# Kernel tuning notes

Measured on AMD Instinct MI355X. Metric: run time of the kernel, lower is better.

## Reference

```python
import jax, jax.numpy as jnp
import numpy as np

B, NI, D, P, R = 32, 1024, 1024, 1000, 3  # batch, patches, d_model, pool_size, agg rounds


def setup_inputs() -> dict:
    key = jax.random.key(0)
    ks = jax.random.split(key, 12)
    w = lambda k, shape: jax.random.normal(k, shape, jnp.float32) * 0.02
    return {
        "att_feats": jax.random.normal(ks[0], (B, NI, D), jnp.float32),
        "fc_feats": jax.random.normal(ks[1], (B, D), jnp.float32),
        "pool": jax.random.normal(ks[2], (P, D), jnp.float32),
        "W_agg": w(ks[3], (R, D, D)),          # stacked agg projections (no bias)
        "Wq": w(ks[4], (D, D)), "bq": jnp.zeros((D,), jnp.float32),
        "Wk": w(ks[5], (D, D)), "bk": jnp.zeros((D,), jnp.float32),
        "Wv": w(ks[6], (D, D)), "bv": jnp.zeros((D,), jnp.float32),
        "Wc": w(ks[7], (D, D)), "bc": jnp.zeros((D,), jnp.float32),
        "Wg": w(ks[8], (2 * D,)), "bg": jnp.asarray(-1.0, jnp.float32),  # gate bias init -1
        "residual_scale": jnp.asarray(0.1, jnp.float32),
    }


def reference(att_feats, fc_feats, pool, W_agg, Wq, bq, Wk, bk, Wv, bv, Wc, bc, Wg, bg, residual_scale):
    d = att_feats.shape[-1]
    scale = 1.0 / jnp.sqrt(jnp.asarray(d, att_feats.dtype))
    v_hat = fc_feats  # fc dim == d_model path

    # Aggregate attention: R rounds over normality pool, averaged (Eq. 4-6)
    q_all = jnp.einsum('bd,rod->rbo', v_hat, W_agg)            # [R,B,D]
    scores = jnp.einsum('rbo,po->rbp', q_all, pool) * scale    # [R,B,P]
    weights = jax.nn.softmax(scores, axis=-1)
    v_agg = jnp.einsum('rbp,pd->bd', weights, pool) / R        # [B,D]

    # Differentiate attention (Eq. 7-10)
    q = v_hat @ Wq.T + bq
    k = v_agg @ Wk.T + bk
    v = v_agg @ Wv.T + bv
    sim = jnp.sum(q * k, axis=-1, keepdims=True) * scale       # [B,1]
    v_common = jax.nn.sigmoid(sim) * v
    v_diff = jax.nn.relu((v_hat - v_common) @ Wc.T + bc)       # [B,D] (dropout = identity, eval)

    # Gated residual; split gate weight to avoid materializing the concat
    Wg1, Wg2 = Wg[:d], Wg[d:]
    g = jax.nn.sigmoid(att_feats @ Wg1 + (v_diff @ Wg2)[:, None] + bg)  # [B,NI]
    return att_feats + residual_scale * g[..., None] * v_diff[:, None, :]
```

## Files before the change

### kernel.cpp

```cpp
#include <hip/hip_runtime.h>

#define D 1024
#define B 32
#define NI 1024
#define PP 1000
#define R 3
#define SPLITS 8
#define VS 8
#define BK 32
#define KT (D / SPLITS / BK)
#define PAD 34

typedef float f32x4_t __attribute__((ext_vector_type(4)));

__device__ __forceinline__ void nt_store4v(float* p, f32x4_t x) {
    __builtin_nontemporal_store(x, (f32x4_t*)p);
}

__device__ __forceinline__ float wred(float x) {
    #pragma unroll
    for (int off = 32; off; off >>= 1) x += __shfl_xor(x, off, 64);
    return x;
}
__device__ __forceinline__ float wmax(float x) {
    #pragma unroll
    for (int off = 32; off; off >>= 1) x = fmaxf(x, __shfl_xor(x, off, 64));
    return x;
}

template<int NXS>
__device__ __forceinline__ void gemm_core(
        const float* __restrict__ A, int mbase, int Mrows,
        const float* __restrict__ Xb, int xrstride, size_t xss,
        int kc0, float acc[4][4]) {
    __shared__ float Ws[128][PAD];
    __shared__ float Xs[32][PAD];
    const int t = threadIdx.x;
    const int ty = t >> 3, tx = t & 7;
    const int m0 = 4 * ty, b0 = 4 * tx;
    const int lrow = t >> 3, lq = t & 7;

    #pragma unroll
    for (int i = 0; i < 4; ++i)
        #pragma unroll
        for (int j = 0; j < 4; ++j) acc[i][j] = 0.f;

    for (int kt = 0; kt < KT; ++kt) {
        const int kc = kc0 + kt * BK;
        #pragma unroll
        for (int rr = 0; rr < 4; ++rr) {
            const int row = lrow + 32 * rr;
            float4 v = make_float4(0.f, 0.f, 0.f, 0.f);
            if (mbase + row < Mrows)
                v = *(const float4*)(A + (size_t)(mbase + row) * D + kc + 4 * lq);
            *(float2*)&Ws[row][4 * lq]     = make_float2(v.x, v.y);
            *(float2*)&Ws[row][4 * lq + 2] = make_float2(v.z, v.w);
        }
        {
            const float* xp = Xb + (size_t)lrow * xrstride + kc + 4 * lq;
            float4 v = *(const float4*)xp;
            #pragma unroll
            for (int s = 1; s < NXS; ++s) {
                float4 w = *(const float4*)(xp + (size_t)s * xss);
                v.x += w.x; v.y += w.y; v.z += w.z; v.w += w.w;
            }
            *(float2*)&Xs[lrow][4 * lq]     = make_float2(v.x, v.y);
            *(float2*)&Xs[lrow][4 * lq + 2] = make_float2(v.z, v.w);
        }
        __syncthreads();
        #pragma unroll
        for (int kp = 0; kp < 16; ++kp) {
            float2 wv[4], xv[4];
            #pragma unroll
            for (int i = 0; i < 4; ++i) wv[i] = *(const float2*)&Ws[m0 + i][2 * kp];
            #pragma unroll
            for (int j = 0; j < 4; ++j) xv[j] = *(const float2*)&Xs[b0 + j][2 * kp];
            #pragma unroll
            for (int i = 0; i < 4; ++i)
                #pragma unroll
                for (int j = 0; j < 4; ++j) {
                    acc[i][j] += wv[i].x * xv[j].x;
                    acc[i][j] += wv[i].y * xv[j].y;
                }
        }
        __syncthreads();
    }
}

__global__ __launch_bounds__(256) void gemm_k1q(const float* __restrict__ Wagg,
        const float* __restrict__ Wq, const float* __restrict__ fc,
        float* __restrict__ qallp, float* __restrict__ qkvp) {
    const int mb = blockIdx.x, s = blockIdx.y;
    const int t = threadIdx.x, ty = t >> 3, tx = t & 7;
    float acc[4][4];
    if (mb < 24) {
        const int mbase = mb * 128;
        gemm_core<1>(Wagg, mbase, R * D, fc, D, 0, s * 128, acc);
        const int m = mbase + 4 * ty;
        #pragma unroll
        for (int j = 0; j < 4; ++j) {
            float* cp = qallp + ((size_t)(s * B) + 4 * tx + j) * (R * D) + m;
            *(float4*)cp = make_float4(acc[0][j], acc[1][j], acc[2][j], acc[3][j]);
        }
    } else {
        const int mbase = (mb - 24) * 128;
        gemm_core<1>(Wq, mbase, D, fc, D, 0, s * 128, acc);
        const int m = mbase + 4 * ty;
        #pragma unroll
        for (int j = 0; j < 4; ++j) {
            float* cp = qkvp + ((size_t)((s * R + 0) * B) + 4 * tx + j) * D + m;
            *(float4*)cp = make_float4(acc[0][j], acc[1][j], acc[2][j], acc[3][j]);
        }
    }
}

__global__ __launch_bounds__(256) void gemm_k2(const float* __restrict__ pool,
        const float* __restrict__ qallp, float* __restrict__ Cp) {
    const int mb = blockIdx.x, s = blockIdx.y, r = blockIdx.z;
    const int mbase = mb * 128;
    float acc[4][4];
    gemm_core<SPLITS>(pool, mbase, PP, qallp + r * D, R * D, (size_t)B * R * D,
                      s * 128, acc);
    const int t = threadIdx.x, ty = t >> 3, tx = t & 7;
    const int m = mbase + 4 * ty;
    if (m >= PP) return;
    #pragma unroll
    for (int j = 0; j < 4; ++j) {
        float* cp = Cp + ((size_t)((s * R + r) * B) + 4 * tx + j) * D + m;
        *(float4*)cp = make_float4(acc[0][j], acc[1][j], acc[2][j], acc[3][j]);
    }
}

__global__ __launch_bounds__(256) void gemm_k5kv(const float* __restrict__ Wk,
        const float* __restrict__ Wv, const float* __restrict__ vaggp,
        float* __restrict__ Cp) {
    const int mb = blockIdx.x, s = blockIdx.y, z = blockIdx.z;
    const int mbase = mb * 128;
    float acc[4][4];
    gemm_core<VS>((z == 0) ? Wk : Wv, mbase, D, vaggp, D, (size_t)B * D,
                  s * 128, acc);
    const int t = threadIdx.x, ty = t >> 3, tx = t & 7;
    const int m = mbase + 4 * ty;
    #pragma unroll
    for (int j = 0; j < 4; ++j) {
        float* cp = Cp + ((size_t)((s * R + z + 1) * B) + 4 * tx + j) * D + m;
        *(float4*)cp = make_float4(acc[0][j], acc[1][j], acc[2][j], acc[3][j]);
    }
}

__global__ __launch_bounds__(256) void gemm_k7(const float* __restrict__ Wc,
        const float* __restrict__ u, float* __restrict__ Cp) {
    const int mb = blockIdx.x, s = blockIdx.y;
    const int mbase = mb * 128;
    float acc[4][4];
    gemm_core<1>(Wc, mbase, D, u, D, 0, s * 128, acc);
    const int t = threadIdx.x, ty = t >> 3, tx = t & 7;
    const int m = mbase + 4 * ty;
    #pragma unroll
    for (int j = 0; j < 4; ++j) {
        float* cp = Cp + ((size_t)(s * B) + 4 * tx + j) * D + m;
        *(float4*)cp = make_float4(acc[0][j], acc[1][j], acc[2][j], acc[3][j]);
    }
}

__global__ __launch_bounds__(256) void k3_wbar(const float* __restrict__ scp,
        float* __restrict__ wbar) {
    const int b = blockIdx.x;
    const int t = threadIdx.x, w = t >> 6, lane = t & 63;
    __shared__ float red[8];
    float wb[4] = {0.f, 0.f, 0.f, 0.f};
    for (int r = 0; r < R; ++r) {
        float v[4];
        float mx = -1e30f;
        #pragma unroll
        for (int i = 0; i < 4; ++i) {
            const int p = t + 256 * i;
            float x = -1e30f;
            if (p < PP) {
                x = 0.f;
                #pragma unroll
                for (int s = 0; s < SPLITS; ++s)
                    x += scp[((size_t)((s * R + r) * B) + b) * D + p];
                x *= 0.03125f;
            }
            v[i] = x;
            mx = fmaxf(mx, x);
        }
        mx = wmax(mx);
        if (lane == 0) red[w] = mx;
        __syncthreads();
        mx = fmaxf(fmaxf(red[0], red[1]), fmaxf(red[2], red[3]));
        float e[4], sum = 0.f;
        #pragma unroll
        for (int i = 0; i < 4; ++i) {
            const int p = t + 256 * i;
            e[i] = (p < PP) ? __expf(v[i] - mx) : 0.f;
            sum += e[i];
        }
        sum = wred(sum);
        if (lane == 0) red[4 + w] = sum;
        __syncthreads();
        const float inv = 1.f / (red[4] + red[5] + red[6] + red[7]);
        #pragma unroll
        for (int i = 0; i < 4; ++i) wb[i] += e[i] * inv;
        __syncthreads();
    }
    #pragma unroll
    for (int i = 0; i < 4; ++i) {
        const int p = t + 256 * i;
        wbar[(size_t)b * 1024 + p] = wb[i] * (1.f / 3.f);
    }
}

__global__ __launch_bounds__(256) void k4_vagg(const float* __restrict__ wbar,
        const float* __restrict__ pool, float* __restrict__ vaggp) {
    const int db = blockIdx.x, ps = blockIdx.y;
    __shared__ float Ps[32][132];
    __shared__ float Wbt[32][36];
    const int t = threadIdx.x;
    const int ty = t >> 3, tx = t & 7;
    float acc[4][4];
    #pragma unroll
    for (int i = 0; i < 4; ++i)
        #pragma unroll
        for (int j = 0; j < 4; ++j) acc[i][j] = 0.f;

    for (int pt = 0; pt < 4; ++pt) {
        const int p0 = ps * 128 + pt * 32;
        {
            const int prow = t >> 5, qc = t & 31;
            #pragma unroll
            for (int rr = 0; rr < 4; ++rr) {
                const int pr = prow + 8 * rr;
                float4 v = make_float4(0.f, 0.f, 0.f, 0.f);
                if (p0 + pr < PP)
                    v = *(const float4*)(pool + (size_t)(p0 + pr) * D + db * 128 + 4 * qc);
                *(float4*)&Ps[pr][4 * qc] = v;
            }
        }
        {
            const int bb = t >> 3, q = t & 7;
            float4 v = *(const float4*)(wbar + (size_t)bb * 1024 + p0 + 4 * q);
            Wbt[4 * q + 0][bb] = v.x; Wbt[4 * q + 1][bb] = v.y;
            Wbt[4 * q + 2][bb] = v.z; Wbt[4 * q + 3][bb] = v.w;
        }
        __syncthreads();
        #pragma unroll
        for (int pg = 0; pg < 8; ++pg) {
            #pragma unroll
            for (int pp = 0; pp < 4; ++pp) {
                const int p = 4 * pg + pp;
                float4 xv = *(const float4*)&Ps[p][4 * ty];
                float4 wv = *(const float4*)&Wbt[p][4 * tx];
                const float xs[4] = {xv.x, xv.y, xv.z, xv.w};
                const float wsv[4] = {wv.x, wv.y, wv.z, wv.w};
                #pragma unroll
                for (int i = 0; i < 4; ++i)
                    #pragma unroll
                    for (int j = 0; j < 4; ++j)
                        acc[i][j] += xs[i] * wsv[j];
            }
        }
        __syncthreads();
    }
    const int dbase = db * 128 + 4 * ty;
    #pragma unroll
    for (int j = 0; j < 4; ++j) {
        float* op = vaggp + ((size_t)ps * B + 4 * tx + j) * D + dbase;
        *(float4*)op = make_float4(acc[0][j], acc[1][j], acc[2][j], acc[3][j]);
    }
}

__global__ __launch_bounds__(256) void k6_u(const float* __restrict__ qkvp,
        const float* __restrict__ bq, const float* __restrict__ bk,
        const float* __restrict__ bv, const float* __restrict__ vhat,
        float* __restrict__ u) {
    const int b = blockIdx.x;
    const int t = threadIdx.x, w = t >> 6, lane = t & 63;
    const int d = 4 * t;
    float4 qv = *(const float4*)(bq + d);
    float4 kv = *(const float4*)(bk + d);
    #pragma unroll
    for (int s = 0; s < SPLITS; ++s) {
        float4 a = *(const float4*)(qkvp + ((size_t)((s * R + 0) * B) + b) * D + d);
        float4 c = *(const float4*)(qkvp + ((size_t)((s * R + 1) * B) + b) * D + d);
        qv.x += a.x; qv.y += a.y; qv.z += a.z; qv.w += a.w;
        kv.x += c.x; kv.y += c.y; kv.z += c.z; kv.w += c.w;
    }
    float local = qv.x * kv.x + qv.y * kv.y + qv.z * kv.z + qv.w * kv.w;
    local = wred(local);
    __shared__ float red[4];
    if (lane == 0) red[w] = local;
    __syncthreads();
    const float sim = (red[0] + red[1] + red[2] + red[3]) * 0.03125f;
    const float sig = 1.f / (1.f + __expf(-sim));
    float4 vv = *(const float4*)(bv + d);
    #pragma unroll
    for (int s = 0; s < SPLITS; ++s) {
        float4 c = *(const float4*)(qkvp + ((size_t)((s * R + 2) * B) + b) * D + d);
        vv.x += c.x; vv.y += c.y; vv.z += c.z; vv.w += c.w;
    }
    const float4 vh = *(const float4*)(vhat + (size_t)b * D + d);
    float4 o;
    o.x = vh.x - sig * vv.x; o.y = vh.y - sig * vv.y;
    o.z = vh.z - sig * vv.z; o.w = vh.w - sig * vv.w;
    *(float4*)(u + (size_t)b * D + d) = o;
}

__global__ __launch_bounds__(256) void k8_cb(const float* __restrict__ vdp,
        const float* __restrict__ bc, const float* __restrict__ Wg,
        const float* __restrict__ bg, float* __restrict__ vdiff,
        float* __restrict__ cb) {
    const int b = blockIdx.x;
    const int t = threadIdx.x, w = t >> 6, lane = t & 63;
    const int d = 4 * t;
    float4 a = *(const float4*)(bc + d);
    #pragma unroll
    for (int s = 0; s < SPLITS; ++s) {
        float4 c = *(const float4*)(vdp + ((size_t)(s * B) + b) * D + d);
        a.x += c.x; a.y += c.y; a.z += c.z; a.w += c.w;
    }
    a.x = fmaxf(a.x, 0.f); a.y = fmaxf(a.y, 0.f);
    a.z = fmaxf(a.z, 0.f); a.w = fmaxf(a.w, 0.f);
    *(float4*)(vdiff + (size_t)b * D + d) = a;
    const float4 g2 = *(const float4*)(Wg + D + d);
    float local = a.x * g2.x + a.y * g2.y + a.z * g2.z + a.w * g2.w;
    local = wred(local);
    __shared__ float red[4];
    if (lane == 0) red[w] = local;
    __syncthreads();
    if (t == 0) cb[b] = red[0] + red[1] + red[2] + red[3] + bg[0];
}

#define LD16(dst, srcp) \
    asm volatile("global_load_dwordx4 %0, %1, off" : "=v"(dst) : "v"(srcp) : "memory")

__global__ __launch_bounds__(256) void k9_main(const float* __restrict__ att,
        const float* __restrict__ Wg, const float* __restrict__ cb,
        const float* __restrict__ vdiff, const float* __restrict__ rs_p,
        float* __restrict__ out) {
    __shared__ float vds[1024];
    const int t = threadIdx.x;
    const int b = blockIdx.x >> 5;
    *(float4*)&vds[4 * t] = *(const float4*)(vdiff + (size_t)b * D + 4 * t);
    __syncthreads();
    const int w = t >> 6, lane = t & 63;
    float4 g[4];
    #pragma unroll
    for (int kk = 0; kk < 4; ++kk)
        g[kk] = *(const float4*)(Wg + 4 * lane + 256 * kk);
    const float rsv = rs_p[0];
    const float cbb = cb[b];
    const size_t row0 = (size_t)blockIdx.x * 32 + w * 8;
    const float* ap = att + row0 * D;
    float* op = out + row0 * D;
    const int co = 4 * lane;

    f32x4_t bufA[8], bufB[8];

#define PAIR_COMPUTE_STORE(BUF, OPB)                                          \
    {                                                                         \
        float acc0 = 0.f, acc1 = 0.f;                                         \
        _Pragma("unroll")                                                     \
        for (int kk = 0; kk < 4; ++kk) {                                      \
            acc0 += BUF[kk][0] * g[kk].x + BUF[kk][1] * g[kk].y +             \
                    BUF[kk][2] * g[kk].z + BUF[kk][3] * g[kk].w;              \
            acc1 += BUF[4 + kk][0] * g[kk].x + BUF[4 + kk][1] * g[kk].y +     \
                    BUF[4 + kk][2] * g[kk].z + BUF[4 + kk][3] * g[kk].w;      \
        }                                                                     \
        _Pragma("unroll")                                                     \
        for (int off = 32; off; off >>= 1) {                                  \
            acc0 += __shfl_xor(acc0, off, 64);                                \
            acc1 += __shfl_xor(acc1, off, 64);                                \
        }                                                                     \
        const float grs0 = rsv / (1.f + __expf(-(acc0 + cbb)));               \
        const float grs1 = rsv / (1.f + __expf(-(acc1 + cbb)));               \
        _Pragma("unroll")                                                     \
        for (int kk = 0; kk < 4; ++kk) {                                      \
            const int col = co + 256 * kk;                                    \
            const float4 vd = *(const float4*)&vds[col];                      \
            f32x4_t o0, o1;                                                   \
            o0[0] = BUF[kk][0] + grs0 * vd.x; o0[1] = BUF[kk][1] + grs0 * vd.y; \
            o0[2] = BUF[kk][2] + grs0 * vd.z; o0[3] = BUF[kk][3] + grs0 * vd.w; \
            o1[0] = BUF[4 + kk][0] + grs1 * vd.x; o1[1] = BUF[4 + kk][1] + grs1 * vd.y; \
            o1[2] = BUF[4 + kk][2] + grs1 * vd.z; o1[3] = BUF[4 + kk][3] + grs1 * vd.w; \
            nt_store4v((OPB) + col, o0);                                      \
            nt_store4v((OPB) + D + col, o1);                                  \
        }                                                                     \
    }

#define ISSUE_PAIR(BUF, ROWOFF)                                               \
    _Pragma("unroll")                                                         \
    for (int q = 0; q < 8; ++q) {                                             \
        const float* _src = ap + (size_t)((ROWOFF) + (q >> 2)) * D + co + 256 * (q & 3); \
        LD16(BUF[q], _src);                                                   \
    }

    ISSUE_PAIR(bufA, 0);
    asm volatile("s_waitcnt vmcnt(0)");
    __builtin_amdgcn_sched_barrier(0);

    ISSUE_PAIR(bufB, 2);
    PAIR_COMPUTE_STORE(bufA, op);

    ISSUE_PAIR(bufA, 4);
    asm volatile("s_waitcnt vmcnt(16)");
    __builtin_amdgcn_sched_barrier(0);
    PAIR_COMPUTE_STORE(bufB, op + 2 * D);

    ISSUE_PAIR(bufB, 6);
    asm volatile("s_waitcnt vmcnt(16)");
    __builtin_amdgcn_sched_barrier(0);
    PAIR_COMPUTE_STORE(bufA, op + 4 * D);

    asm volatile("s_waitcnt vmcnt(8)");
    __builtin_amdgcn_sched_barrier(0);
    PAIR_COMPUTE_STORE(bufB, op + 6 * D);
}

extern "C" void kernel_launch(void* const* d_in, const int* in_sizes, int n_in,
                              void* d_out, int out_size, void* d_ws, size_t ws_size,
                              hipStream_t stream) {
    const float* att  = (const float*)d_in[0];
    const float* fc   = (const float*)d_in[1];
    const float* pool = (const float*)d_in[2];
    const float* Wagg = (const float*)d_in[3];
    const float* Wq   = (const float*)d_in[4];
    const float* bq   = (const float*)d_in[5];
    const float* Wk   = (const float*)d_in[6];
    const float* bk   = (const float*)d_in[7];
    const float* Wv   = (const float*)d_in[8];
    const float* bv   = (const float*)d_in[9];
    const float* Wc   = (const float*)d_in[10];
    const float* bc   = (const float*)d_in[11];
    const float* Wg   = (const float*)d_in[12];
    const float* bg   = (const float*)d_in[13];
    const float* rs   = (const float*)d_in[14];
    float* out = (float*)d_out;

    float* ws = (float*)d_ws;
    float* qallp = ws;
    float* scp   = qallp + (size_t)SPLITS * B * R * D;
    float* wbar  = scp + (size_t)SPLITS * R * B * D;
    float* vaggp = wbar + (size_t)B * 1024;
    float* qkvp  = vaggp + (size_t)VS * B * D;
    float* ub    = qkvp + (size_t)SPLITS * R * B * D;
    float* vdp   = ub + (size_t)B * D;
    float* vdiff = vdp + (size_t)SPLITS * B * D;
    float* cbuf  = vdiff + (size_t)B * D;

    gemm_k1q<<<dim3(32, SPLITS), 256, 0, stream>>>(Wagg, Wq, fc, qallp, qkvp);
    gemm_k2<<<dim3(8, SPLITS, R), 256, 0, stream>>>(pool, qallp, scp);
    k3_wbar<<<B, 256, 0, stream>>>(scp, wbar);
    k4_vagg<<<dim3(8, VS), 256, 0, stream>>>(wbar, pool, vaggp);
    gemm_k5kv<<<dim3(8, SPLITS, 2), 256, 0, stream>>>(Wk, Wv, vaggp, qkvp);
    k6_u<<<B, 256, 0, stream>>>(qkvp, bq, bk, bv, fc, ub);
    gemm_k7<<<dim3(8, SPLITS), 256, 0, stream>>>(Wc, ub, vdp);
    k8_cb<<<B, 256, 0, stream>>>(vdp, bc, Wg, bg, vdiff, cbuf);
    k9_main<<<B * 32, 256, 0, stream>>>(att, Wg, cbuf, vdiff, rs, out);
}
```

Measured before the change: 129.8 us.

## Distribute Wc over v_hat minus sigmoid-scaled v to remove a dependent kernel

Uses linearity, Wc(v_hat - sig*v) = Wc v_hat - sig*Wc v, to split the last projection. Wc·v_hat is now computed early alongside the first GEMM, and Wc·v is computed straight from the split-K V partials plus bias. The sigmoid scaling, bias, relu and gate reduction are applied in one small epilogue kernel, which removes the separate k6_u launch from the serial chain. The cost is extra GEMM work (a second Wc product) and more partial-sum traffic.

```diff
diff --git a/kernel.cpp b/kernel.cpp
--- a/kernel.cpp
+++ b/kernel.cpp
@@ -28,11 +28,11 @@
     return x;
 }
 
-template<int NXS>
+template<int NXS, bool XB = false>
 __device__ __forceinline__ void gemm_core(
         const float* __restrict__ A, int mbase, int Mrows,
         const float* __restrict__ Xb, int xrstride, size_t xss,
-        int kc0, float acc[4][4]) {
+        int kc0, float acc[4][4], const float* __restrict__ xbias = nullptr) {
     __shared__ float Ws[128][PAD];
     __shared__ float Xs[32][PAD];
     const int t = threadIdx.x;
@@ -64,6 +64,10 @@
                 float4 w = *(const float4*)(xp + (size_t)s * xss);
                 v.x += w.x; v.y += w.y; v.z += w.z; v.w += w.w;
             }
+            if constexpr (XB) {
+                float4 bb = *(const float4*)(xbias + kc + 4 * lq);
+                v.x += bb.x; v.y += bb.y; v.z += bb.z; v.w += bb.w;
+            }
             *(float2*)&Xs[lrow][4 * lq]     = make_float2(v.x, v.y);
             *(float2*)&Xs[lrow][4 * lq + 2] = make_float2(v.z, v.w);
         }
@@ -88,8 +92,9 @@
 }
 
 __global__ __launch_bounds__(256) void gemm_k1q(const float* __restrict__ Wagg,
-        const float* __restrict__ Wq, const float* __restrict__ fc,
-        float* __restrict__ qallp, float* __restrict__ qkvp) {
+        const float* __restrict__ Wq, const float* __restrict__ Wc,
+        const float* __restrict__ fc, float* __restrict__ qallp,
+        float* __restrict__ qkvp, float* __restrict__ avhp) {
     const int mb = blockIdx.x, s = blockIdx.y;
     const int t = threadIdx.x, ty = t >> 3, tx = t & 7;
     float acc[4][4];
@@ -102,13 +107,22 @@
             float* cp = qallp + ((size_t)(s * B) + 4 * tx + j) * (R * D) + m;
             *(float4*)cp = make_float4(acc[0][j], acc[1][j], acc[2][j], acc[3][j]);
         }
-    } else {
+    } else if (mb < 32) {
         const int mbase = (mb - 24) * 128;
         gemm_core<1>(Wq, mbase, D, fc, D, 0, s * 128, acc);
         const int m = mbase + 4 * ty;
         #pragma unroll
         for (int j = 0; j < 4; ++j) {
             float* cp = qkvp + ((size_t)((s * R + 0) * B) + 4 * tx + j) * D + m;
+            *(float4*)cp = make_float4(acc[0][j], acc[1][j], acc[2][j], acc[3][j]);
+        }
+    } else {
+        const int mbase = (mb - 32) * 128;
+        gemm_core<1>(Wc, mbase, D, fc, D, 0, s * 128, acc);
+        const int m = mbase + 4 * ty;
+        #pragma unroll
+        for (int j = 0; j < 4; ++j) {
+            float* cp = avhp + ((size_t)(s * B) + 4 * tx + j) * D + m;
             *(float4*)cp = make_float4(acc[0][j], acc[1][j], acc[2][j], acc[3][j]);
         }
     }
@@ -148,12 +162,14 @@
     }
 }
 
-__global__ __launch_bounds__(256) void gemm_k7(const float* __restrict__ Wc,
-        const float* __restrict__ u, float* __restrict__ Cp) {
+__global__ __launch_bounds__(256) void gemm_k7v(const float* __restrict__ Wc,
+        const float* __restrict__ qkvp, const float* __restrict__ bv,
+        float* __restrict__ Cp) {
     const int mb = blockIdx.x, s = blockIdx.y;
     const int mbase = mb * 128;
     float acc[4][4];
-    gemm_core<1>(Wc, mbase, D, u, D, 0, s * 128, acc);
+    gemm_core<SPLITS, true>(Wc, mbase, D, qkvp + (size_t)2 * B * D, D,
+                            (size_t)R * B * D, s * 128, acc, bv);
     const int t = threadIdx.x, ty = t >> 3, tx = t & 7;
     const int m = mbase + 4 * ty;
     #pragma unroll
@@ -271,63 +287,54 @@
     }
 }
 
-__global__ __launch_bounds__(256) void k6_u(const float* __restrict__ qkvp,
+__global__ __launch_bounds__(256) void k8_new(const float* __restrict__ qkvp,
         const float* __restrict__ bq, const float* __restrict__ bk,
-        const float* __restrict__ bv, const float* __restrict__ vhat,
-        float* __restrict__ u) {
-    const int b = blockIdx.x;
-    const int t = threadIdx.x, w = t >> 6, lane = t & 63;
-    const int d = 4 * t;
-    float4 qv = *(const float4*)(bq + d);
-    float4 kv = *(const float4*)(bk + d);
-    #pragma unroll
-    for (int s = 0; s < SPLITS; ++s) {
-        float4 a = *(const float4*)(qkvp + ((size_t)((s * R + 0) * B) + b) * D + d);
-        float4 c = *(const float4*)(qkvp + ((size_t)((s * R + 1) * B) + b) * D + d);
-        qv.x += a.x; qv.y += a.y; qv.z += a.z; qv.w += a.w;
-        kv.x += c.x; kv.y += c.y; kv.z += c.z; kv.w += c.w;
-    }
-    float local = qv.x * kv.x + qv.y * kv.y + qv.z * kv.z + qv.w * kv.w;
-    local = wred(local);
-    __shared__ float red[4];
-    if (lane == 0) red[w] = local;
-    __syncthreads();
-    const float sim = (red[0] + red[1] + red[2] + red[3]) * 0.03125f;
-    const float sig = 1.f / (1.f + __expf(-sim));
-    float4 vv = *(const float4*)(bv + d);
-    #pragma unroll
-    for (int s = 0; s < SPLITS; ++s) {
-        float4 c = *(const float4*)(qkvp + ((size_t)((s * R + 2) * B) + b) * D + d);
-        vv.x += c.x; vv.y += c.y; vv.z += c.z; vv.w += c.w;
-    }
-    const float4 vh = *(const float4*)(vhat + (size_t)b * D + d);
-    float4 o;
-    o.x = vh.x - sig * vv.x; o.y = vh.y - sig * vv.y;
-    o.z = vh.z - sig * vv.z; o.w = vh.w - sig * vv.w;
-    *(float4*)(u + (size_t)b * D + d) = o;
-}
-
-__global__ __launch_bounds__(256) void k8_cb(const float* __restrict__ vdp,
+        const float* __restrict__ avhp, const float* __restrict__ wcvp,
         const float* __restrict__ bc, const float* __restrict__ Wg,
         const float* __restrict__ bg, float* __restrict__ vdiff,
         float* __restrict__ cb) {
     const int b = blockIdx.x;
     const int t = threadIdx.x, w = t >> 6, lane = t & 63;
     const int d = 4 * t;
-    float4 a = *(const float4*)(bc + d);
+    __shared__ float red[4];
+    float4 qv = *(const float4*)(bq + d);
+    float4 kv = *(const float4*)(bk + d);
     #pragma unroll
     for (int s = 0; s < SPLITS; ++s) {
-        float4 c = *(const float4*)(vdp + ((size_t)(s * B) + b) * D + d);
-        a.x += c.x; a.y += c.y; a.z += c.z; a.w += c.w;
-    }
-    a.x = fmaxf(a.x, 0.f); a.y = fmaxf(a.y, 0.f);
-    a.z = fmaxf(a.z, 0.f); a.w = fmaxf(a.w, 0.f);
-    *(float4*)(vdiff + (size_t)b * D + d) = a;
+        float4 a = *(const float4*)(qkvp + ((size_t)((s * R + 0) * B) + b) * D + d);
+        float4 c = *(const float4*)(qkvp + ((size_t)((s * R + 1) * B) + b) * D + d);
+        qv.x += a.x; qv.y += a.y; qv.z += a.z; qv.w += a.w;
+        kv.x += c.x; kv.y += c.y; kv.z += c.z; kv.w += c.w;
+    }
+    float local = qv.x * kv.x + qv.y * kv.y + qv.z * kv.z + qv.w * kv.w;
+    local = wred(local);
+    if (lane == 0) red[w] = local;
+    __syncthreads();
+    const float sim = (red[0] + red[1] + red[2] + red[3]) * 0.03125f;
+    const float sig = 1.f / (1.f + __expf(-sim));
+
+    float4 av = make_float4(0.f, 0.f, 0.f, 0.f);
+    float4 wc = make_float4(0.f, 0.f, 0.f, 0.f);
+    #pragma unroll
+    for (int s = 0; s < SPLITS; ++s) {
+        float4 a = *(const float4*)(avhp + ((size_t)(s * B) + b) * D + d);
+        float4 c = *(const float4*)(wcvp + ((size_t)(s * B) + b) * D + d);
+        av.x += a.x; av.y += a.y; av.z += a.z; av.w += a.w;
+        wc.x += c.x; wc.y += c.y; wc.z += c.z; wc.w += c.w;
+    }
+    const float4 bcv = *(const float4*)(bc + d);
+    float4 vd;
+    vd.x = fmaxf(av.x - sig * wc.x + bcv.x, 0.f);
+    vd.y = fmaxf(av.y - sig * wc.y + bcv.y, 0.f);
+    vd.z = fmaxf(av.z - sig * wc.z + bcv.z, 0.f);
+    vd.w = fmaxf(av.w - sig * wc.w + bcv.w, 0.f);
+    *(float4*)(vdiff + (size_t)b * D + d) = vd;
+
     const float4 g2 = *(const float4*)(Wg + D + d);
-    float local = a.x * g2.x + a.y * g2.y + a.z * g2.z + a.w * g2.w;
-    local = wred(local);
-    __shared__ float red[4];
-    if (lane == 0) red[w] = local;
+    float local2 = vd.x * g2.x + vd.y * g2.y + vd.z * g2.z + vd.w * g2.w;
+    local2 = wred(local2);
+    __syncthreads();
+    if (lane == 0) red[w] = local2;
     __syncthreads();
     if (t == 0) cb[b] = red[0] + red[1] + red[2] + red[3] + bg[0];
 }
@@ -444,18 +451,19 @@
     float* wbar  = scp + (size_t)SPLITS * R * B * D;
     float* vaggp = wbar + (size_t)B * 1024;
     float* qkvp  = vaggp + (size_t)VS * B * D;
-    float* ub    = qkvp + (size_t)SPLITS * R * B * D;
-    float* vdp   = ub + (size_t)B * D;
-    float* vdiff = vdp + (size_t)SPLITS * B * D;
+    float* avhp  = qkvp + (size_t)SPLITS * R * B * D;
+    float* wcvp  = avhp + (size_t)SPLITS * B * D;
+    float* vdiff = wcvp + (size_t)SPLITS * B * D;
     float* cbuf  = vdiff + (size_t)B * D;
 
-    gemm_k1q<<<dim3(32, SPLITS), 256, 0, stream>>>(Wagg, Wq, fc, qallp, qkvp);
+    gemm_k1q<<<dim3(40, SPLITS), 256, 0, stream>>>(Wagg, Wq, Wc, fc,
+                                                   qallp, qkvp, avhp);
     gemm_k2<<<dim3(8, SPLITS, R), 256, 0, stream>>>(pool, qallp, scp);
     k3_wbar<<<B, 256, 0, stream>>>(scp, wbar);
     k4_vagg<<<dim3(8, VS), 256, 0, stream>>>(wbar, pool, vaggp);
     gemm_k5kv<<<dim3(8, SPLITS, 2), 256, 0, stream>>>(Wk, Wv, vaggp, qkvp);
-    k6_u<<<B, 256, 0, stream>>>(qkvp, bq, bk, bv, fc, ub);
-    gemm_k7<<<dim3(8, SPLITS), 256, 0, stream>>>(Wc, ub, vdp);
-    k8_cb<<<B, 256, 0, stream>>>(vdp, bc, Wg, bg, vdiff, cbuf);
+    gemm_k7v<<<dim3(8, SPLITS), 256, 0, stream>>>(Wc, qkvp, bv, wcvp);
+    k8_new<<<B, 256, 0, stream>>>(qkvp, bq, bk, avhp, wcvp, bc, Wg, bg,
+                                  vdiff, cbuf);
     k9_main<<<B * 32, 256, 0, stream>>>(att, Wg, cbuf, vdiff, rs, out);
 }
```

Result: no change. 132.0 us (+1.7%).
